# Kernel tuning notes

Hardware: AMD Instinct MI355X
Metric: run time of the kernel (lower is better)

## Reference

```python
import jax, jax.numpy as jnp
import numpy as np

DIM = 512
GLBL = 108
N = 100000
NUM_SEGMENTS = 1024


def setup_inputs() -> dict:
    key = jax.random.key(0)
    ks = jax.random.split(key, 9)
    x = jax.random.normal(ks[0], (N, DIM), dtype=jnp.float32)
    glbl_x = jax.random.normal(ks[1], (N, GLBL), dtype=jnp.float32)
    batch = jnp.sort(jax.random.randint(ks[2], (N,), 0, NUM_SEGMENTS, dtype=jnp.int32))
    # MLP params: (dim+108 -> dim), (dim -> dim), (dim -> 1)
    s0 = 1.0 / np.sqrt(DIM + GLBL)
    s1 = 1.0 / np.sqrt(DIM)
    W0 = jax.random.uniform(ks[3], (DIM + GLBL, DIM), jnp.float32, -s0, s0)
    b0 = jax.random.uniform(ks[4], (DIM,), jnp.float32, -s0, s0)
    W1 = jax.random.uniform(ks[5], (DIM, DIM), jnp.float32, -s1, s1)
    b1 = jax.random.uniform(ks[6], (DIM,), jnp.float32, -s1, s1)
    W2 = jax.random.uniform(ks[7], (DIM, 1), jnp.float32, -s1, s1)
    b2 = jax.random.uniform(ks[8], (1,), jnp.float32, -s1, s1)
    return {"x": x, "batch": batch, "glbl_x": glbl_x,
            "W0": W0, "b0": b0, "W1": W1, "b1": b1, "W2": W2, "b2": b2}


def segment_softmax(logits, seg, num_segments):
    # logits: [N, 1]; per-segment numerically-stable softmax (torch_geometric softmax)
    m = jax.ops.segment_max(logits, seg, num_segments=num_segments)  # [G, 1]
    e = jnp.exp(logits - m[seg])
    s = jax.ops.segment_sum(e, seg, num_segments=num_segments)       # [G, 1]
    return e / (s[seg] + 1e-16)


def reference(x, batch, glbl_x, W0, b0, W1, b1, W2, b2):
    out = jnp.concatenate([x, glbl_x], axis=-1)          # [N, dim+108]
    out = jax.nn.softplus(out @ W0 + b0)                 # [N, dim]
    out = jax.nn.softplus(out @ W1 + b1)                 # [N, dim]
    out = out @ W2 + b2                                  # [N, 1]
    return segment_softmax(out, batch, NUM_SEGMENTS)     # [N, 1]
```

## Files before the change

### kernel.cpp

```cpp
#include <hip/hip_runtime.h>
#include <hip/hip_bf16.h>
#include <math.h>


#define NSEG 1024

typedef __attribute__((ext_vector_type(8))) short short8;
typedef __attribute__((ext_vector_type(4))) float f32x4;

__device__ __forceinline__ unsigned short f2bf(float f) {
  __hip_bfloat16 h = __float2bfloat16(f);
  return *reinterpret_cast<unsigned short*>(&h);
}
__device__ __forceinline__ float softplus_fast(float z) {
  float t = __expf(-fabsf(z));
  return fmaxf(z, 0.f) + __logf(1.f + t);
}
__device__ __forceinline__ void gll16(const unsigned short* g, unsigned short* l) {
  __builtin_amdgcn_global_load_lds(
      (const __attribute__((address_space(1))) void*)g,
      (__attribute__((address_space(3))) void*)l, 16, 0, 0);
}
__device__ __forceinline__ int xcd_swz(int bid, int nwg) {
  int q = nwg >> 3, r = nwg & 7, x = bid & 7, i = bid >> 3;
  return (x < r ? x * (q + 1) : r * (q + 1) + (x - r) * q) + i;
}

__global__ __launch_bounds__(256) void prep(const float* __restrict__ W0,
                                            const float* __restrict__ W1,
                                            unsigned short* __restrict__ W0T,
                                            unsigned short* __restrict__ W1T,
                                            float* __restrict__ logits, int Mp) {
  int t = blockIdx.x * 256 + threadIdx.x;
  if (t < 512 * 640) {
    int n = t / 640, k = t % 640;
    W0T[t] = f2bf(k < 620 ? W0[(size_t)k * 512 + n] : 0.f);
    return;
  }
  t -= 512 * 640;
  if (t < 512 * 512) {
    int n = t / 512, k = t % 512;
    W1T[t] = f2bf(W1[(size_t)k * 512 + n]);
    return;
  }
  t -= 512 * 512;
  if (t < Mp) logits[t] = 0.f;
}

__global__ __launch_bounds__(256) void pack_a0(const float* __restrict__ x,
                                               const float* __restrict__ gx,
                                               unsigned short* __restrict__ A0,
                                               int N, int Mp) {
  int t = blockIdx.x * 256 + threadIdx.x;
  if (t >= Mp * 80) return;
  int row = t / 80, c = t % 80;
  union { unsigned short u[8]; uint4 q; } v;
  if (row >= N) {
#pragma unroll
    for (int j = 0; j < 8; ++j) v.u[j] = 0;
  } else if (c < 64) {
    const float4* p = (const float4*)(x + (size_t)row * 512 + c * 8);
    float4 a = p[0], b = p[1];
    v.u[0] = f2bf(a.x); v.u[1] = f2bf(a.y); v.u[2] = f2bf(a.z); v.u[3] = f2bf(a.w);
    v.u[4] = f2bf(b.x); v.u[5] = f2bf(b.y); v.u[6] = f2bf(b.z); v.u[7] = f2bf(b.w);
  } else {
#pragma unroll
    for (int j = 0; j < 8; ++j) {
      int col = c * 8 + j;
      float f = (col < 620) ? gx[(size_t)row * 108 + (col - 512)] : 0.f;
      v.u[j] = f2bf(f);
    }
  }
  *reinterpret_cast<uint4*>(A0 + (size_t)row * 640 + c * 8) = v.q;
}

template <int K, bool FUSE>
__global__ __launch_bounds__(256, 3) void gemm_bf16(const unsigned short* __restrict__ A,
                                                    const unsigned short* __restrict__ WT,
                                                    const float* __restrict__ bias,
                                                    unsigned short* __restrict__ C,
                                                    const float* __restrict__ W2,
                                                    float* __restrict__ logits, int nwg) {
  constexpr int KT = K / 32;
  __shared__ unsigned short As[2][128 * 32];
  __shared__ unsigned short Ws[2][128 * 32];
  const int L = xcd_swz(blockIdx.x, nwg);
  const int nt = L & 3, mt = L >> 2;
  const int tid = threadIdx.x, lane = tid & 63, wid = tid >> 6;
  const int wm = wid >> 1, wn = wid & 1, lm = lane & 15, rch = lane >> 4;

  const unsigned short* Ag = A + (size_t)(mt * 128) * K;
  const unsigned short* Wg = WT + (size_t)(nt * 128) * K;

  f32x4 acc[4][4] = {};

  auto stage = [&](int buf, int kb) {
#pragma unroll
    for (int i2 = 0; i2 < 2; ++i2) {
      int f = i2 * 256 + tid;
      int row = f >> 2;
      int sc = ((f & 3) ^ ((row >> 1) & 3)) << 3;
      gll16(Ag + (size_t)row * K + kb + sc, &As[buf][f * 8]);
      gll16(Wg + (size_t)row * K + kb + sc, &Ws[buf][f * 8]);
    }
  };

  stage(0, 0);

  for (int kt = 0; kt < KT; ++kt) {
    const int cur = kt & 1;
    __syncthreads();
    if (kt + 1 < KT) stage(cur ^ 1, (kt + 1) * 32);

    short8 af[4], wf[4];
#pragma unroll
    for (int mi = 0; mi < 4; ++mi) {
      int rw = wm * 64 + mi * 16 + lm;
      af[mi] = *reinterpret_cast<const short8*>(
          &As[cur][rw * 32 + ((rch ^ ((rw >> 1) & 3)) << 3)]);
    }
#pragma unroll
    for (int ni = 0; ni < 4; ++ni) {
      int rw = wn * 64 + ni * 16 + lm;
      wf[ni] = *reinterpret_cast<const short8*>(
          &Ws[cur][rw * 32 + ((rch ^ ((rw >> 1) & 3)) << 3)]);
    }
    __builtin_amdgcn_s_setprio(1);
#pragma unroll
    for (int mi = 0; mi < 4; ++mi)
#pragma unroll
      for (int ni = 0; ni < 4; ++ni)
        acc[mi][ni] = __builtin_amdgcn_mfma_f32_16x16x32_bf16(wf[ni], af[mi], acc[mi][ni], 0, 0, 0);
    __builtin_amdgcn_s_setprio(0);
  }

#pragma unroll
  for (int mi = 0; mi < 4; ++mi) {
    const int m = mt * 128 + wm * 64 + mi * 16 + lm;
    float part = 0.f;
#pragma unroll
    for (int ni = 0; ni < 4; ++ni) {
      const int n0 = nt * 128 + wn * 64 + ni * 16 + (rch << 2);
      const f32x4 bb = *reinterpret_cast<const f32x4*>(bias + n0);
      f32x4 v = acc[mi][ni];
      if constexpr (!FUSE) {
        union { unsigned short u[4]; uint2 qv; } o;
#pragma unroll
        for (int rr = 0; rr < 4; ++rr) o.u[rr] = f2bf(softplus_fast(v[rr] + bb[rr]));
        *reinterpret_cast<uint2*>(C + (size_t)m * 512 + n0) = o.qv;
      } else {
        const f32x4 wv = *reinterpret_cast<const f32x4*>(W2 + n0);
#pragma unroll
        for (int rr = 0; rr < 4; ++rr) part += softplus_fast(v[rr] + bb[rr]) * wv[rr];
      }
    }
    if constexpr (FUSE) {
      part += __shfl_xor(part, 16);
      part += __shfl_xor(part, 32);
      if (lane < 16) atomicAdd(logits + m, part);
    }
  }
}

__global__ __launch_bounds__(256) void segsoftmax(const float* __restrict__ logits,
                                                  const int* __restrict__ batch,
                                                  float* __restrict__ out, int N) {
  const int g = blockIdx.x;
  const int tid = threadIdx.x;
  int lo = 0, hi = N;
  while (lo < hi) { int mid = (lo + hi) >> 1; if (batch[mid] < g) lo = mid + 1; else hi = mid; }
  const int beg = lo;
  hi = N;
  while (lo < hi) { int mid = (lo + hi) >> 1; if (batch[mid] < g + 1) lo = mid + 1; else hi = mid; }
  const int end = lo;
  if (beg >= end) return;

  __shared__ float sh[4];
  float m = -INFINITY;
  for (int i = beg + tid; i < end; i += 256) m = fmaxf(m, logits[i]);
#pragma unroll
  for (int o = 32; o; o >>= 1) m = fmaxf(m, __shfl_down(m, o));
  if ((tid & 63) == 0) sh[tid >> 6] = m;
  __syncthreads();
  m = fmaxf(fmaxf(sh[0], sh[1]), fmaxf(sh[2], sh[3]));
  __syncthreads();

  float s = 0.f;
  for (int i = beg + tid; i < end; i += 256) s += expf(logits[i] - m);
#pragma unroll
  for (int o = 32; o; o >>= 1) s += __shfl_down(s, o);
  if ((tid & 63) == 0) sh[tid >> 6] = s;
  __syncthreads();
  s = sh[0] + sh[1] + sh[2] + sh[3];

  const float inv = 1.f / (s + 1e-16f);
  for (int i = beg + tid; i < end; i += 256) out[i] = expf(logits[i] - m) * inv;
}

extern "C" void kernel_launch(void* const* d_in, const int* in_sizes, int n_in,
                              void* d_out, int out_size, void* d_ws, size_t ws_size,
                              hipStream_t stream) {
  const float* x = (const float*)d_in[0];
  const int* batch = (const int*)d_in[1];
  const float* gx = (const float*)d_in[2];
  const float* W0 = (const float*)d_in[3];
  const float* b0 = (const float*)d_in[4];
  const float* W1 = (const float*)d_in[5];
  const float* b1 = (const float*)d_in[6];
  const float* W2 = (const float*)d_in[7];
  float* out = (float*)d_out;

  const int N = in_sizes[1];
  const int Mp = ((N + 127) / 128) * 128;
  const int nwg = (Mp / 128) * 4;

  auto align256 = [](size_t v) { return (v + 255) & ~(size_t)255; };
  char* ws = (char*)d_ws;
  size_t off = 0;
  unsigned short* A0 = (unsigned short*)(ws + off);  off = align256(off + (size_t)Mp * 640 * 2);
  unsigned short* W0T = (unsigned short*)(ws + off); off = align256(off + (size_t)512 * 640 * 2);
  unsigned short* W1T = (unsigned short*)(ws + off); off = align256(off + (size_t)512 * 512 * 2);
  unsigned short* H0 = (unsigned short*)(ws + off);  off = align256(off + (size_t)Mp * 512 * 2);
  float* logits = (float*)(ws + off);                off = align256(off + (size_t)Mp * 4);
  (void)ws_size; (void)n_in; (void)out_size;

  const int prep_elems = 512 * 640 + 512 * 512 + Mp;
  prep<<<(prep_elems + 255) / 256, 256, 0, stream>>>(W0, W1, W0T, W1T, logits, Mp);
  pack_a0<<<(Mp * 80 + 255) / 256, 256, 0, stream>>>(x, gx, A0, N, Mp);

  gemm_bf16<640, false><<<nwg, 256, 0, stream>>>(A0, W0T, b0, H0, nullptr, nullptr, nwg);
  gemm_bf16<512, true><<<nwg, 256, 0, stream>>>(H0, W1T, b1, nullptr, W2, logits, nwg);

  segsoftmax<<<NSEG, 256, 0, stream>>>(logits, batch, out, N);
}
```

Measured before the change: 311.9 us.

## Split weight transpose via LDS, vectorize glbl pack, register-direct first GEMM

Replaces the strided per-element weight transpose with a tiled LDS transpose, splits the A0 packing so the 108-wide global features load as float4 vectors, and folds logits zeroing into pack_a0. The first GEMM becomes a register-fed kernel with no LDS: each wave loads MFMA fragments straight from global memory with double-buffered register chunks over a 64x256 tile. The second GEMM is specialised with higher occupancy bounds. The register-direct loads give up LDS sharing, so each block relies on cache for reuse of A and W.

```diff
diff --git a/kernel.cpp b/kernel.cpp
--- a/kernel.cpp
+++ b/kernel.cpp
@@ -16,7 +16,7 @@
   float t = __expf(-fabsf(z));
   return fmaxf(z, 0.f) + __logf(1.f + t);
 }
-__device__ __forceinline__ void gll16(const unsigned short* g, unsigned short* l) {
+__device__ __forceinline__ void gll16(const void* g, void* l) {
   __builtin_amdgcn_global_load_lds(
       (const __attribute__((address_space(1))) void*)g,
       (__attribute__((address_space(3))) void*)l, 16, 0, 0);
@@ -26,62 +26,158 @@
   return (x < r ? x * (q + 1) : r * (q + 1) + (x - r) * q) + i;
 }
 
-__global__ __launch_bounds__(256) void prep(const float* __restrict__ W0,
-                                            const float* __restrict__ W1,
-                                            unsigned short* __restrict__ W0T,
-                                            unsigned short* __restrict__ W1T,
-                                            float* __restrict__ logits, int Mp) {
-  int t = blockIdx.x * 256 + threadIdx.x;
-  if (t < 512 * 640) {
-    int n = t / 640, k = t % 640;
-    W0T[t] = f2bf(k < 620 ? W0[(size_t)k * 512 + n] : 0.f);
-    return;
-  }
-  t -= 512 * 640;
-  if (t < 512 * 512) {
-    int n = t / 512, k = t % 512;
-    W1T[t] = f2bf(W1[(size_t)k * 512 + n]);
-    return;
-  }
-  t -= 512 * 512;
-  if (t < Mp) logits[t] = 0.f;
+template <int KDIM, int KOUT>
+__global__ __launch_bounds__(256) void transposeW(const float* __restrict__ W,
+                                                  unsigned short* __restrict__ WT) {
+  __shared__ float lds[64][65];
+  const int bk = blockIdx.x >> 3, bn = blockIdx.x & 7;
+  const int k0 = bk * 64, n0 = bn * 64;
+  const int tid = threadIdx.x;
+#pragma unroll
+  for (int i2 = 0; i2 < 4; ++i2) {
+    int f = i2 * 256 + tid;
+    int row = f >> 4, q = f & 15;
+    int k = k0 + row;
+    float4 v = float4{0.f, 0.f, 0.f, 0.f};
+    if (k < KDIM) v = *reinterpret_cast<const float4*>(W + (size_t)k * 512 + n0 + q * 4);
+    lds[row][q * 4 + 0] = v.x; lds[row][q * 4 + 1] = v.y;
+    lds[row][q * 4 + 2] = v.z; lds[row][q * 4 + 3] = v.w;
+  }
+  __syncthreads();
+#pragma unroll
+  for (int i3 = 0; i3 < 2; ++i3) {
+    int f = i3 * 256 + tid;
+    int row2 = f >> 3, q2 = f & 7;
+    union { unsigned short u[8]; uint4 qv; } o;
+#pragma unroll
+    for (int j = 0; j < 8; ++j) o.u[j] = f2bf(lds[q2 * 8 + j][row2]);
+    *reinterpret_cast<uint4*>(WT + (size_t)(n0 + row2) * KOUT + k0 + q2 * 8) = o.qv;
+  }
 }
 
 __global__ __launch_bounds__(256) void pack_a0(const float* __restrict__ x,
                                                const float* __restrict__ gx,
                                                unsigned short* __restrict__ A0,
+                                               float* __restrict__ logits,
                                                int N, int Mp) {
   int t = blockIdx.x * 256 + threadIdx.x;
-  if (t >= Mp * 80) return;
-  int row = t / 80, c = t % 80;
   union { unsigned short u[8]; uint4 q; } v;
-  if (row >= N) {
-#pragma unroll
-    for (int j = 0; j < 8; ++j) v.u[j] = 0;
-  } else if (c < 64) {
-    const float4* p = (const float4*)(x + (size_t)row * 512 + c * 8);
-    float4 a = p[0], b = p[1];
-    v.u[0] = f2bf(a.x); v.u[1] = f2bf(a.y); v.u[2] = f2bf(a.z); v.u[3] = f2bf(a.w);
-    v.u[4] = f2bf(b.x); v.u[5] = f2bf(b.y); v.u[6] = f2bf(b.z); v.u[7] = f2bf(b.w);
-  } else {
-#pragma unroll
-    for (int j = 0; j < 8; ++j) {
-      int col = c * 8 + j;
-      float f = (col < 620) ? gx[(size_t)row * 108 + (col - 512)] : 0.f;
-      v.u[j] = f2bf(f);
-    }
-  }
-  *reinterpret_cast<uint4*>(A0 + (size_t)row * 640 + c * 8) = v.q;
-}
-
-template <int K, bool FUSE>
-__global__ __launch_bounds__(256, 3) void gemm_bf16(const unsigned short* __restrict__ A,
-                                                    const unsigned short* __restrict__ WT,
-                                                    const float* __restrict__ bias,
-                                                    unsigned short* __restrict__ C,
-                                                    const float* __restrict__ W2,
-                                                    float* __restrict__ logits, int nwg) {
-  constexpr int KT = K / 32;
+  if (t < Mp * 64) {
+    int row = t >> 6, c = t & 63;
+    if (row >= N) {
+#pragma unroll
+      for (int j = 0; j < 8; ++j) v.u[j] = 0;
+    } else {
+      const float4* p = (const float4*)(x + (size_t)row * 512 + c * 8);
+      float4 a = p[0], b = p[1];
+      v.u[0] = f2bf(a.x); v.u[1] = f2bf(a.y); v.u[2] = f2bf(a.z); v.u[3] = f2bf(a.w);
+      v.u[4] = f2bf(b.x); v.u[5] = f2bf(b.y); v.u[6] = f2bf(b.z); v.u[7] = f2bf(b.w);
+    }
+    *reinterpret_cast<uint4*>(A0 + (size_t)row * 640 + c * 8) = v.q;
+    return;
+  }
+  t -= Mp * 64;
+  if (t < Mp * 16) {
+    int row = t >> 4, j = t & 15;
+    if (row >= N || j >= 14) {
+#pragma unroll
+      for (int k = 0; k < 8; ++k) v.u[k] = 0;
+    } else if (j <= 12) {
+      const float4* p = (const float4*)(gx + (size_t)row * 108 + j * 8);
+      float4 a = p[0], b = p[1];
+      v.u[0] = f2bf(a.x); v.u[1] = f2bf(a.y); v.u[2] = f2bf(a.z); v.u[3] = f2bf(a.w);
+      v.u[4] = f2bf(b.x); v.u[5] = f2bf(b.y); v.u[6] = f2bf(b.z); v.u[7] = f2bf(b.w);
+    } else {
+      const float4* p = (const float4*)(gx + (size_t)row * 108 + 104);
+      float4 a = p[0];
+      v.u[0] = f2bf(a.x); v.u[1] = f2bf(a.y); v.u[2] = f2bf(a.z); v.u[3] = f2bf(a.w);
+      v.u[4] = 0; v.u[5] = 0; v.u[6] = 0; v.u[7] = 0;
+    }
+    *reinterpret_cast<uint4*>(A0 + (size_t)row * 640 + 512 + j * 8) = v.q;
+    return;
+  }
+  t -= Mp * 16;
+  if (t < Mp) logits[t] = 0.f;
+}
+
+#define LOAD_CHUNK(ab, wb, kb_)                                      \
+  {                                                                  \
+    ab[0] = *reinterpret_cast<const short8*>(aP0 + (kb_));           \
+    ab[1] = *reinterpret_cast<const short8*>(aP1 + (kb_));           \
+    ab[2] = *reinterpret_cast<const short8*>(aP2 + (kb_));           \
+    ab[3] = *reinterpret_cast<const short8*>(aP3 + (kb_));           \
+    wb[0] = *reinterpret_cast<const short8*>(wP0 + (kb_));           \
+    wb[1] = *reinterpret_cast<const short8*>(wP1 + (kb_));           \
+    wb[2] = *reinterpret_cast<const short8*>(wP2 + (kb_));           \
+    wb[3] = *reinterpret_cast<const short8*>(wP3 + (kb_));           \
+  }
+#define MFMA_CHUNK(ab, wb)                                                        \
+  {                                                                               \
+    _Pragma("unroll") for (int mi = 0; mi < 4; ++mi)                              \
+      _Pragma("unroll") for (int ni = 0; ni < 4; ++ni)                            \
+        acc[mi][ni] =                                                             \
+            __builtin_amdgcn_mfma_f32_16x16x32_bf16(wb[ni], ab[mi], acc[mi][ni],  \
+                                                    0, 0, 0);                     \
+  }
+
+__global__ __launch_bounds__(256, 3) void gemm0_rf(const unsigned short* __restrict__ A0,
+                                                   const unsigned short* __restrict__ W0T,
+                                                   const float* __restrict__ b0,
+                                                   unsigned short* __restrict__ H0,
+                                                   int nwg) {
+  constexpr int K = 640, KT = 20;
+  const int L = xcd_swz(blockIdx.x, nwg);
+  const int nt = L & 1, mt = L >> 1;
+  const int tid = threadIdx.x, lane = tid & 63, wid = tid >> 6;
+  const int lm = lane & 15, rch = lane >> 4;
+  const int rowbase = mt * 64;
+  const int colbase = nt * 256 + wid * 64;
+
+  const unsigned short* aP0 = A0 + (size_t)(rowbase + 0 * 16 + lm) * K + rch * 8;
+  const unsigned short* aP1 = A0 + (size_t)(rowbase + 1 * 16 + lm) * K + rch * 8;
+  const unsigned short* aP2 = A0 + (size_t)(rowbase + 2 * 16 + lm) * K + rch * 8;
+  const unsigned short* aP3 = A0 + (size_t)(rowbase + 3 * 16 + lm) * K + rch * 8;
+  const unsigned short* wP0 = W0T + (size_t)(colbase + 0 * 16 + lm) * K + rch * 8;
+  const unsigned short* wP1 = W0T + (size_t)(colbase + 1 * 16 + lm) * K + rch * 8;
+  const unsigned short* wP2 = W0T + (size_t)(colbase + 2 * 16 + lm) * K + rch * 8;
+  const unsigned short* wP3 = W0T + (size_t)(colbase + 3 * 16 + lm) * K + rch * 8;
+
+  f32x4 acc[4][4] = {};
+  short8 ab0[4], wb0[4], ab1[4], wb1[4];
+
+  LOAD_CHUNK(ab0, wb0, 0);
+  LOAD_CHUNK(ab1, wb1, 32);
+
+#pragma unroll
+  for (int kt = 0; kt < KT; kt += 2) {
+    MFMA_CHUNK(ab0, wb0);
+    if (kt + 2 < KT) LOAD_CHUNK(ab0, wb0, (kt + 2) * 32);
+    MFMA_CHUNK(ab1, wb1);
+    if (kt + 3 < KT) LOAD_CHUNK(ab1, wb1, (kt + 3) * 32);
+  }
+
+#pragma unroll
+  for (int mi = 0; mi < 4; ++mi) {
+    const int m = rowbase + mi * 16 + lm;
+#pragma unroll
+    for (int ni = 0; ni < 4; ++ni) {
+      const int n0 = colbase + ni * 16 + (rch << 2);
+      const f32x4 bb = *reinterpret_cast<const f32x4*>(b0 + n0);
+      f32x4 v = acc[mi][ni];
+      union { unsigned short u[4]; uint2 qv; } o;
+#pragma unroll
+      for (int rr = 0; rr < 4; ++rr) o.u[rr] = f2bf(softplus_fast(v[rr] + bb[rr]));
+      *reinterpret_cast<uint2*>(H0 + (size_t)m * 512 + n0) = o.qv;
+    }
+  }
+}
+
+__global__ __launch_bounds__(256, 4) void gemm1(const unsigned short* __restrict__ H0,
+                                                const unsigned short* __restrict__ W1T,
+                                                const float* __restrict__ b1,
+                                                const float* __restrict__ W2,
+                                                float* __restrict__ logits, int nwg) {
+  constexpr int K = 512, KT = 16;
   __shared__ unsigned short As[2][128 * 32];
   __shared__ unsigned short Ws[2][128 * 32];
   const int L = xcd_swz(blockIdx.x, nwg);
@@ -89,8 +185,8 @@
   const int tid = threadIdx.x, lane = tid & 63, wid = tid >> 6;
   const int wm = wid >> 1, wn = wid & 1, lm = lane & 15, rch = lane >> 4;
 
-  const unsigned short* Ag = A + (size_t)(mt * 128) * K;
-  const unsigned short* Wg = WT + (size_t)(nt * 128) * K;
+  const unsigned short* Ag = H0 + (size_t)(mt * 128) * K;
+  const unsigned short* Wg = W1T + (size_t)(nt * 128) * K;
 
   f32x4 acc[4][4] = {};
 
@@ -141,24 +237,15 @@
 #pragma unroll
     for (int ni = 0; ni < 4; ++ni) {
       const int n0 = nt * 128 + wn * 64 + ni * 16 + (rch << 2);
-      const f32x4 bb = *reinterpret_cast<const f32x4*>(bias + n0);
+      const f32x4 bb = *reinterpret_cast<const f32x4*>(b1 + n0);
+      const f32x4 wv = *reinterpret_cast<const f32x4*>(W2 + n0);
       f32x4 v = acc[mi][ni];
-      if constexpr (!FUSE) {
-        union { unsigned short u[4]; uint2 qv; } o;
-#pragma unroll
-        for (int rr = 0; rr < 4; ++rr) o.u[rr] = f2bf(softplus_fast(v[rr] + bb[rr]));
-        *reinterpret_cast<uint2*>(C + (size_t)m * 512 + n0) = o.qv;
-      } else {
-        const f32x4 wv = *reinterpret_cast<const f32x4*>(W2 + n0);
-#pragma unroll
-        for (int rr = 0; rr < 4; ++rr) part += softplus_fast(v[rr] + bb[rr]) * wv[rr];
-      }
-    }
-    if constexpr (FUSE) {
-      part += __shfl_xor(part, 16);
-      part += __shfl_xor(part, 32);
-      if (lane < 16) atomicAdd(logits + m, part);
-    }
+#pragma unroll
+      for (int rr = 0; rr < 4; ++rr) part += softplus_fast(v[rr] + bb[rr]) * wv[rr];
+    }
+    part += __shfl_xor(part, 16);
+    part += __shfl_xor(part, 32);
+    if (lane < 16) atomicAdd(logits + m, part);
   }
 }
 
@@ -212,7 +299,8 @@
 
   const int N = in_sizes[1];
   const int Mp = ((N + 127) / 128) * 128;
-  const int nwg = (Mp / 128) * 4;
+  const int nwg0 = (Mp / 64) * 2;
+  const int nwg1 = (Mp / 128) * 4;
 
   auto align256 = [](size_t v) { return (v + 255) & ~(size_t)255; };
   char* ws = (char*)d_ws;
@@ -224,12 +312,12 @@
   float* logits = (float*)(ws + off);                off = align256(off + (size_t)Mp * 4);
   (void)ws_size; (void)n_in; (void)out_size;
 
-  const int prep_elems = 512 * 640 + 512 * 512 + Mp;
-  prep<<<(prep_elems + 255) / 256, 256, 0, stream>>>(W0, W1, W0T, W1T, logits, Mp);
-  pack_a0<<<(Mp * 80 + 255) / 256, 256, 0, stream>>>(x, gx, A0, N, Mp);
-
-  gemm_bf16<640, false><<<nwg, 256, 0, stream>>>(A0, W0T, b0, H0, nullptr, nullptr, nwg);
-  gemm_bf16<512, true><<<nwg, 256, 0, stream>>>(H0, W1T, b1, nullptr, W2, logits, nwg);
+  transposeW<620, 640><<<80, 256, 0, stream>>>(W0, W0T);
+  transposeW<512, 512><<<64, 256, 0, stream>>>(W1, W1T);
+  pack_a0<<<((size_t)Mp * 81 + 255) / 256, 256, 0, stream>>>(x, gx, A0, logits, N, Mp);
+
+  gemm0_rf<<<nwg0, 256, 0, stream>>>(A0, W0T, b0, H0, nwg0);
+  gemm1<<<nwg1, 256, 0, stream>>>(H0, W1T, b1, W2, logits, nwg1);
 
   segsoftmax<<<NSEG, 256, 0, stream>>>(logits, batch, out, N);
 }
```

New measurement: 436.7 us. 1.4x slower.
